# Performance work log

Hardware: AMD Instinct MI355X
Metric: run time of the kernel (lower is better)

The kernel has to match this reference:

```python
import jax, jax.numpy as jnp
import numpy as np

B, S, D, H = 2, 2048, 1024, 16
HD = D // H
SCALE = HD ** -0.5

def setup_inputs() -> dict:
    key = jax.random.key(0)
    ks = jax.random.split(key, 3)
    x = jax.random.normal(ks[0], (B, S, D), dtype=jnp.float32)
    Wqkv = jax.random.normal(ks[1], (D, 3 * D), dtype=jnp.float32) * (D ** -0.5)
    bqkv = jnp.zeros((3 * D,), dtype=jnp.float32)
    Wproj = jax.random.normal(ks[2], (D, D), dtype=jnp.float32) * (D ** -0.5)
    bproj = jnp.zeros((D,), dtype=jnp.float32)
    return {"x": x, "Wqkv": Wqkv, "bqkv": bqkv, "Wproj": Wproj, "bproj": bproj}

def reference(x, Wqkv, bqkv, Wproj, bproj):
    b, s, d = x.shape
    qkv = x @ Wqkv + bqkv                       # (b, s, 3d)
    qkv = qkv.reshape(b, s, 3, H, HD)
    q, k, v = (qkv[:, :, 0], qkv[:, :, 1], qkv[:, :, 2])  # (b, s, h, hd)
    # scores: (b, h, s, s)
    attn = jnp.einsum('bqhd,bkhd->bhqk', q, k) * SCALE
    attn = jax.nn.softmax(attn, axis=-1)
    out = jnp.einsum('bhqk,bkhd->bqhd', attn, v).reshape(b, s, d)
    out = out @ Wproj + bproj
    return out
```

## Files before the change

kernel.cpp:

```cpp
#include <hip/hip_runtime.h>

typedef __attribute__((ext_vector_type(8))) short bf16x8;
typedef __attribute__((ext_vector_type(4))) float f32x4;
typedef __attribute__((ext_vector_type(16))) float f32x16;
typedef unsigned short u16;
typedef unsigned int u32;

#define MFMA16(a,b,c) __builtin_amdgcn_mfma_f32_16x16x32_bf16((a),(b),(c),0,0,0)
#define MFMA32(a,b,c) __builtin_amdgcn_mfma_f32_32x32x16_bf16((a),(b),(c),0,0,0)

#if __has_builtin(__builtin_amdgcn_exp2f)
#define EXP2(x) __builtin_amdgcn_exp2f(x)
#else
#define EXP2(x) __expf((x) * 0.6931471805599453f)
#endif

__device__ __forceinline__ u16 f2bf(float f) {
  u32 u = __builtin_bit_cast(u32, f);
  u += 0x7FFFu + ((u >> 16) & 1u);
  return (u16)(u >> 16);
}

__device__ __forceinline__ u32 cvtpk(float lo, float hi) {
  u32 r;
  asm("v_cvt_pk_bf16_f32 %0, %1, %2" : "=v"(r) : "v"(lo), "v"(hi));
  return r;
}

__device__ __forceinline__ void gload16(const u16* g, u16* l) {
  __builtin_amdgcn_global_load_lds(
      (const __attribute__((address_space(1))) u32*)(const void*)g,
      (__attribute__((address_space(3))) u32*)(void*)l, 16, 0, 0);
}

__device__ __forceinline__ bf16x8 ldsfrag(const u16* lds, int row, int chunk) {
  return *(const bf16x8*)(lds + row * 64 + ((chunk ^ (row & 7)) << 3));
}

__global__ __launch_bounds__(256) void convert_x(const float* __restrict__ in,
                                                 u16* __restrict__ out, int n4) {
  int i = blockIdx.x * blockDim.x + threadIdx.x;
  int stride = gridDim.x * blockDim.x;
  for (; i < n4; i += stride) {
    float4 v = ((const float4*)in)[i];
    u32 lo = (u32)f2bf(v.x) | ((u32)f2bf(v.y) << 16);
    u32 hi = (u32)f2bf(v.z) | ((u32)f2bf(v.w) << 16);
    uint2 pv; pv.x = lo; pv.y = hi;
    ((uint2*)out)[i] = pv;
  }
}

__global__ __launch_bounds__(256) void transpose_w(const float* __restrict__ in,
                                                   u16* __restrict__ out,
                                                   int R, int C) {
  __shared__ float t[32][33];
  int c0 = blockIdx.x * 32, r0 = blockIdx.y * 32;
  int tc = threadIdx.x & 31, tr = threadIdx.x >> 5;
#pragma unroll
  for (int j = 0; j < 4; ++j) {
    int r = tr + j * 8;
    t[r][tc] = in[(size_t)(r0 + r) * C + c0 + tc];
  }
  __syncthreads();
#pragma unroll
  for (int j = 0; j < 4; ++j) {
    int cc = tr + j * 8;
    out[(size_t)(c0 + cc) * R + r0 + tc] = f2bf(t[tc][cc]);
  }
}

template <int MODE>
__global__ __launch_bounds__(256) void gemm_k(
    const u16* __restrict__ A, const u16* __restrict__ Bt,
    const float* __restrict__ bias,
    u16* __restrict__ Qo, u16* __restrict__ Ko, u16* __restrict__ Vt,
    float* __restrict__ Of) {
  __shared__ alignas(16) u16 As[2][128 * 32];
  __shared__ alignas(16) u16 Bs[2][128 * 32];
  const int tid = threadIdx.x;
  const int wid = tid >> 6, lane = tid & 63;
  const int g = lane >> 4, lr = lane & 15;
  const int m0 = blockIdx.y * 128, n0 = blockIdx.x * 128;
  const int wr = (wid >> 1) * 64, wc = (wid & 1) * 64;

  f32x4 acc[4][4];
#pragma unroll
  for (int i = 0; i < 4; ++i)
#pragma unroll
    for (int j = 0; j < 4; ++j) acc[i][j] = (f32x4){0.f, 0.f, 0.f, 0.f};

  const u16* Ab = A + (size_t)m0 * 1024;
  const u16* Bb = Bt + (size_t)n0 * 1024;

  const int srow = tid >> 2, sc = tid & 3;
  auto stage = [&](int buf, int kt) {
#pragma unroll
    for (int i = 0; i < 2; ++i) {
      int s = tid + i * 256;
      int row = srow + i * 64, c = sc;
      gload16(Ab + (size_t)row * 1024 + kt + c * 8, As[buf] + s * 8);
      gload16(Bb + (size_t)row * 1024 + kt + c * 8, Bs[buf] + s * 8);
    }
  };

  stage(0, 0);
  __syncthreads();
  int cur = 0;
  for (int kt = 0; kt < 1024; kt += 32) {
    if (kt + 32 < 1024) stage(cur ^ 1, kt + 32);
    bf16x8 af[4], bfr[4];
#pragma unroll
    for (int i = 0; i < 4; ++i)
      af[i] = *(const bf16x8*)(As[cur] + (wr + i * 16 + lr) * 32 + g * 8);
#pragma unroll
    for (int j = 0; j < 4; ++j)
      bfr[j] = *(const bf16x8*)(Bs[cur] + (wc + j * 16 + lr) * 32 + g * 8);
    __builtin_amdgcn_s_setprio(1);
#pragma unroll
    for (int i = 0; i < 4; ++i)
#pragma unroll
      for (int j = 0; j < 4; ++j)
        acc[i][j] = MFMA16(af[i], bfr[j], acc[i][j]);
    __builtin_amdgcn_s_setprio(0);
    __syncthreads();
    cur ^= 1;
  }

  if constexpr (MODE == 1) {
#pragma unroll
    for (int i = 0; i < 4; ++i) {
      int row = m0 + wr + i * 16 + g * 4;
#pragma unroll
      for (int j = 0; j < 4; ++j) {
        int col = n0 + wc + j * 16 + lr;
        float bv = bias[col];
#pragma unroll
        for (int r = 0; r < 4; ++r)
          Of[(size_t)(row + r) * 1024 + col] = acc[i][j][r] + bv;
      }
    }
  } else {
    const int sel = n0 >> 10;
#pragma unroll
    for (int i = 0; i < 4; ++i) {
      int row = m0 + wr + i * 16 + g * 4;
      int b = row >> 11, s = row & 2047;
#pragma unroll
      for (int j = 0; j < 4; ++j) {
        int col = n0 + wc + j * 16 + lr;
        float bv = bias[col];
        int nn = col & 1023;
        int h = nn >> 6, hd = nn & 63;
        if (sel == 2) {
          u16 pk[4];
#pragma unroll
          for (int r = 0; r < 4; ++r) pk[r] = f2bf(acc[i][j][r] + bv);
          uint2 pv;
          pv.x = (u32)pk[0] | ((u32)pk[1] << 16);
          pv.y = (u32)pk[2] | ((u32)pk[3] << 16);
          *(uint2*)(Vt + (size_t)((b * 16 + h) * 64 + hd) * 2048 + s) = pv;
        } else {
          u16* dst = (sel == 0) ? Qo : Ko;
#pragma unroll
          for (int r = 0; r < 4; ++r)
            dst[(size_t)((b * 16 + h) * 2048 + s + r) * 64 + hd] =
                f2bf(acc[i][j][r] + bv);
        }
      }
    }
  }
}

__global__ __launch_bounds__(256, 2) void attn_k(const u16* __restrict__ Q,
                                                 const u16* __restrict__ K,
                                                 const u16* __restrict__ Vt,
                                                 u16* __restrict__ O) {
  __shared__ alignas(16) u16 Ks[3][4096];
  __shared__ alignas(16) u16 Vs[3][4096];
  __shared__ alignas(16) u32 Ps[4 * 1024];
  const int tid = threadIdx.x;
  const int wid = tid >> 6, lane = tid & 63;
  const int l31 = lane & 31, b5 = lane >> 5;
  const int p = blockIdx.x;
  const int l = (p & 7) * 64 + (p >> 3);
  const int qt = l & 15, bh = l >> 4;
  const u16* Qh = Q + (size_t)bh * 2048 * 64;
  const u16* Kh = K + (size_t)bh * 2048 * 64;
  const u16* Vh = Vt + (size_t)bh * 64 * 2048;

  const int qbase = qt * 128 + wid * 32;
  const u16* qp = Qh + (size_t)(qbase + l31) * 64 + b5 * 8;
  bf16x8 qf[4];
#pragma unroll
  for (int c = 0; c < 4; ++c) qf[c] = *(const bf16x8*)(qp + 16 * c);
  __builtin_amdgcn_sched_barrier(0);

  auto stage = [&](int buf, int t) {
#pragma unroll
    for (int i = 0; i < 2; ++i) {
      int s = tid + i * 256;
      int row = s >> 3, c = (s & 7) ^ (row & 7);
      gload16(Kh + (t * 64 + row) * 64 + c * 8, Ks[buf] + s * 8);
      gload16(Vh + row * 2048 + t * 64 + c * 8, Vs[buf] + s * 8);
    }
  };
  stage(0, 0);
  stage(1, 1);

  u32* pw = Ps + wid * 1024 + l31 * 32;
  const int swz = (l31 & 7) << 2;

  f32x16 accO0, accO1;
#pragma unroll
  for (int r = 0; r < 16; ++r) { accO0[r] = 0.f; accO1[r] = 0.f; }
  float mraw = -1e30f;
  float mC = 0.f;
  float lsum = 0.f;

  const float C2 = 0.125f * 1.44269504088896f;

  int cur = 0;
  for (int t = 0; t < 32; ++t) {
    if (t + 2 < 32) {
      int nxt = cur + 2; if (nxt >= 3) nxt -= 3;
      stage(nxt, t + 2);
    }
    if (t < 30)       asm volatile("s_waitcnt vmcnt(8)" ::: "memory");
    else if (t == 30) asm volatile("s_waitcnt vmcnt(4)" ::: "memory");
    else              asm volatile("s_waitcnt vmcnt(0)" ::: "memory");
    __builtin_amdgcn_sched_barrier(0);
    __builtin_amdgcn_s_barrier();
    __builtin_amdgcn_sched_barrier(0);

    const u16* Kc = Ks[cur];
    const u16* Vc = Vs[cur];

    f32x16 s0, s1;
#pragma unroll
    for (int r = 0; r < 16; ++r) { s0[r] = 0.f; s1[r] = 0.f; }
    __builtin_amdgcn_s_setprio(1);
#pragma unroll
    for (int c = 0; c < 4; ++c) {
      bf16x8 k0 = ldsfrag(Kc, l31, 2 * c + b5);
      bf16x8 k1 = ldsfrag(Kc, 32 + l31, 2 * c + b5);
      s0 = MFMA32(k0, qf[c], s0);
      s1 = MFMA32(k1, qf[c], s1);
    }
    __builtin_amdgcn_s_setprio(0);

    float rmax;
    {
      float a0 = fmaxf(fmaxf(s0[0], s0[1]), fmaxf(s0[2], s0[3]));
      float a1 = fmaxf(fmaxf(s0[4], s0[5]), fmaxf(s0[6], s0[7]));
      float a2 = fmaxf(fmaxf(s0[8], s0[9]), fmaxf(s0[10], s0[11]));
      float a3 = fmaxf(fmaxf(s0[12], s0[13]), fmaxf(s0[14], s0[15]));
      float b0 = fmaxf(fmaxf(s1[0], s1[1]), fmaxf(s1[2], s1[3]));
      float b1 = fmaxf(fmaxf(s1[4], s1[5]), fmaxf(s1[6], s1[7]));
      float b2 = fmaxf(fmaxf(s1[8], s1[9]), fmaxf(s1[10], s1[11]));
      float b3 = fmaxf(fmaxf(s1[12], s1[13]), fmaxf(s1[14], s1[15]));
      rmax = fmaxf(fmaxf(fmaxf(a0, a1), fmaxf(a2, a3)),
                   fmaxf(fmaxf(b0, b1), fmaxf(b2, b3)));
    }
    rmax = fmaxf(rmax, __shfl_xor(rmax, 32));

    if (__any(rmax > mraw + 64.f)) {
      float mn = fmaxf(mraw, rmax);
      float al = EXP2((mraw - mn) * C2);
      mraw = mn;
      mC = mn * C2;
      lsum *= al;
#pragma unroll
      for (int r = 0; r < 16; ++r) {
        float ar = __shfl(al, (r & 3) + 8 * (r >> 2) + 4 * b5);
        accO0[r] *= ar;
        accO1[r] *= ar;
      }
    }

    u32 w0[8], w1[8];
#pragma unroll
    for (int i = 0; i < 8; ++i) {
      float p0 = EXP2(__builtin_fmaf(s0[2 * i], C2, -mC));
      float p1 = EXP2(__builtin_fmaf(s0[2 * i + 1], C2, -mC));
      float p2 = EXP2(__builtin_fmaf(s1[2 * i], C2, -mC));
      float p3 = EXP2(__builtin_fmaf(s1[2 * i + 1], C2, -mC));
      lsum += (p0 + p1) + (p2 + p3);
      w0[i] = cvtpk(p0, p1);
      w1[i] = cvtpk(p2, p3);
    }
#pragma unroll
    for (int j = 0; j < 4; ++j) {
      uint2 a; a.x = w0[2 * j]; a.y = w0[2 * j + 1];
      uint2 b; b.x = w1[2 * j]; b.y = w1[2 * j + 1];
      *(uint2*)(pw + ((4 * j + 2 * b5) ^ swz)) = a;
      *(uint2*)(pw + ((16 + 4 * j + 2 * b5) ^ swz)) = b;
    }

    __builtin_amdgcn_s_setprio(1);
#pragma unroll
    for (int c = 0; c < 4; ++c) {
      bf16x8 pf = *(const bf16x8*)(pw + ((8 * c + 4 * b5) ^ swz));
      bf16x8 v0 = ldsfrag(Vc, l31, 2 * c + b5);
      bf16x8 v1 = ldsfrag(Vc, 32 + l31, 2 * c + b5);
      accO0 = MFMA32(pf, v0, accO0);
      accO1 = MFMA32(pf, v1, accO1);
    }
    __builtin_amdgcn_s_setprio(0);

    __builtin_amdgcn_s_barrier();
    __builtin_amdgcn_sched_barrier(0);
    cur += 1; if (cur >= 3) cur -= 3;
  }

  float ls = lsum + __shfl_xor(lsum, 32);
  float inv = 1.f / ls;
  const int b = bh >> 4, h = bh & 15;
#pragma unroll
  for (int r = 0; r < 16; ++r) {
    float ir = __shfl(inv, (r & 3) + 8 * (r >> 2) + 4 * b5);
    int qr = qbase + (r & 3) + 8 * (r >> 2) + 4 * b5;
    size_t rowoff = (size_t)(b * 2048 + qr) * 1024 + h * 64;
    O[rowoff + l31] = f2bf(accO0[r] * ir);
    O[rowoff + 32 + l31] = f2bf(accO1[r] * ir);
  }
}

extern "C" void kernel_launch(void* const* d_in, const int* in_sizes, int n_in,
                              void* d_out, int out_size, void* d_ws, size_t ws_size,
                              hipStream_t stream) {
  (void)in_sizes; (void)n_in; (void)out_size; (void)ws_size;
  const float* x = (const float*)d_in[0];
  const float* Wqkv = (const float*)d_in[1];
  const float* bqkv = (const float*)d_in[2];
  const float* Wproj = (const float*)d_in[3];
  const float* bproj = (const float*)d_in[4];
  float* out = (float*)d_out;

  char* ws = (char*)d_ws;
  size_t off = 0;
  auto alloc = [&](size_t bytes) {
    void* p = ws + off;
    off += (bytes + 255) & ~(size_t)255;
    return p;
  };
  u16* xb     = (u16*)alloc((size_t)4096 * 1024 * 2);
  u16* Wqkvt  = (u16*)alloc((size_t)3072 * 1024 * 2);
  u16* Wprojt = (u16*)alloc((size_t)1024 * 1024 * 2);
  u16* Qb     = (u16*)alloc((size_t)32 * 2048 * 64 * 2);
  u16* Kb     = (u16*)alloc((size_t)32 * 2048 * 64 * 2);
  u16* Vtb    = (u16*)alloc((size_t)32 * 64 * 2048 * 2);
  u16* AOb    = (u16*)alloc((size_t)4096 * 1024 * 2);

  convert_x<<<2048, 256, 0, stream>>>(x, xb, 4096 * 1024 / 4);
  transpose_w<<<dim3(96, 32), 256, 0, stream>>>(Wqkv, Wqkvt, 1024, 3072);
  transpose_w<<<dim3(32, 32), 256, 0, stream>>>(Wproj, Wprojt, 1024, 1024);
  gemm_k<0><<<dim3(24, 32), 256, 0, stream>>>(xb, Wqkvt, bqkv, Qb, Kb, Vtb, nullptr);
  attn_k<<<512, 256, 0, stream>>>(Qb, Kb, Vtb, AOb);
  gemm_k<1><<<dim3(8, 32), 256, 0, stream>>>(AOb, Wprojt, bproj, nullptr, nullptr, nullptr, out);
}
```

Before: 131.0 us.

## Triple-buffer GEMM K-loop with vmcnt waits; pad attention P scratch instead of XOR swizzle

The GEMM kernel moves from double to triple buffering of its A/B tiles. It prefetches two stages ahead, uses explicit vmcnt waits and raw barriers instead of __syncthreads, and sets launch bounds to 3 blocks per CU, so global loads overlap more with MFMA work. In the attention kernel, the P scratch buffer drops its XOR swizzle for row padding (34-word stride) and reads P fragments as two 8-byte loads. This raises GEMM LDS use per block and splits each 16-byte LDS read into two, which may cost LDS bandwidth.

```diff
diff --git a/kernel.cpp b/kernel.cpp
--- a/kernel.cpp
+++ b/kernel.cpp
@@ -70,13 +70,13 @@
 }
 
 template <int MODE>
-__global__ __launch_bounds__(256) void gemm_k(
+__global__ __launch_bounds__(256, 3) void gemm_k(
     const u16* __restrict__ A, const u16* __restrict__ Bt,
     const float* __restrict__ bias,
     u16* __restrict__ Qo, u16* __restrict__ Ko, u16* __restrict__ Vt,
     float* __restrict__ Of) {
-  __shared__ alignas(16) u16 As[2][128 * 32];
-  __shared__ alignas(16) u16 Bs[2][128 * 32];
+  __shared__ alignas(16) u16 As[3][4096];
+  __shared__ alignas(16) u16 Bs[3][4096];
   const int tid = threadIdx.x;
   const int wid = tid >> 6, lane = tid & 63;
   const int g = lane >> 4, lr = lane & 15;
@@ -97,17 +97,27 @@
 #pragma unroll
     for (int i = 0; i < 2; ++i) {
       int s = tid + i * 256;
-      int row = srow + i * 64, c = sc;
-      gload16(Ab + (size_t)row * 1024 + kt + c * 8, As[buf] + s * 8);
-      gload16(Bb + (size_t)row * 1024 + kt + c * 8, Bs[buf] + s * 8);
+      int row = srow + i * 64;
+      gload16(Ab + (size_t)row * 1024 + kt + sc * 8, As[buf] + s * 8);
+      gload16(Bb + (size_t)row * 1024 + kt + sc * 8, Bs[buf] + s * 8);
     }
   };
 
   stage(0, 0);
-  __syncthreads();
+  stage(1, 32);
   int cur = 0;
-  for (int kt = 0; kt < 1024; kt += 32) {
-    if (kt + 32 < 1024) stage(cur ^ 1, kt + 32);
+  for (int ki = 0; ki < 32; ++ki) {
+    if (ki + 2 < 32) {
+      int nxt = cur + 2; if (nxt >= 3) nxt -= 3;
+      stage(nxt, (ki + 2) * 32);
+    }
+    if (ki < 30)       asm volatile("s_waitcnt vmcnt(8)" ::: "memory");
+    else if (ki == 30) asm volatile("s_waitcnt vmcnt(4)" ::: "memory");
+    else               asm volatile("s_waitcnt vmcnt(0)" ::: "memory");
+    __builtin_amdgcn_sched_barrier(0);
+    __builtin_amdgcn_s_barrier();
+    __builtin_amdgcn_sched_barrier(0);
+
     bf16x8 af[4], bfr[4];
 #pragma unroll
     for (int i = 0; i < 4; ++i)
@@ -122,8 +132,10 @@
       for (int j = 0; j < 4; ++j)
         acc[i][j] = MFMA16(af[i], bfr[j], acc[i][j]);
     __builtin_amdgcn_s_setprio(0);
-    __syncthreads();
-    cur ^= 1;
+
+    __builtin_amdgcn_s_barrier();
+    __builtin_amdgcn_sched_barrier(0);
+    cur += 1; if (cur >= 3) cur -= 3;
   }
 
   if constexpr (MODE == 1) {
@@ -177,7 +189,7 @@
                                                  u16* __restrict__ O) {
   __shared__ alignas(16) u16 Ks[3][4096];
   __shared__ alignas(16) u16 Vs[3][4096];
-  __shared__ alignas(16) u32 Ps[4 * 1024];
+  __shared__ alignas(16) u32 Ps[4 * 1088];
   const int tid = threadIdx.x;
   const int wid = tid >> 6, lane = tid & 63;
   const int l31 = lane & 31, b5 = lane >> 5;
@@ -207,8 +219,7 @@
   stage(0, 0);
   stage(1, 1);
 
-  u32* pw = Ps + wid * 1024 + l31 * 32;
-  const int swz = (l31 & 7) << 2;
+  u32* pw = Ps + wid * 1088 + l31 * 34;
 
   f32x16 accO0, accO1;
 #pragma unroll
@@ -292,14 +303,17 @@
     for (int j = 0; j < 4; ++j) {
       uint2 a; a.x = w0[2 * j]; a.y = w0[2 * j + 1];
       uint2 b; b.x = w1[2 * j]; b.y = w1[2 * j + 1];
-      *(uint2*)(pw + ((4 * j + 2 * b5) ^ swz)) = a;
-      *(uint2*)(pw + ((16 + 4 * j + 2 * b5) ^ swz)) = b;
+      *(uint2*)(pw + 4 * j + 2 * b5) = a;
+      *(uint2*)(pw + 16 + 4 * j + 2 * b5) = b;
     }
 
     __builtin_amdgcn_s_setprio(1);
 #pragma unroll
     for (int c = 0; c < 4; ++c) {
-      bf16x8 pf = *(const bf16x8*)(pw + ((8 * c + 4 * b5) ^ swz));
+      uint2 qa = *(const uint2*)(pw + 8 * c + 4 * b5);
+      uint2 qb = *(const uint2*)(pw + 8 * c + 4 * b5 + 2);
+      uint4 u; u.x = qa.x; u.y = qa.y; u.z = qb.x; u.w = qb.y;
+      bf16x8 pf = __builtin_bit_cast(bf16x8, u);
       bf16x8 v0 = ldsfrag(Vc, l31, 2 * c + b5);
       bf16x8 v1 = ldsfrag(Vc, 32 + l31, 2 * c + b5);
       accO0 = MFMA32(pf, v0, accO0);
```

New measurement: 132.6 us. No clear change (+1.2%).
